# Optimization experiments

Hardware: AMD Instinct MI355X
Metric: run time of the kernel (lower is better)

Reference implementation:

```python
import jax, jax.numpy as jnp
import numpy as np

EPS = 1e-12  # torch F.normalize eps
NUM_HEADS = 4
DT = 0.25
NUM_STEPS = 4


def _l2norm(x, axis=-1):
    n = jnp.sqrt(jnp.sum(x * x, axis=axis, keepdims=True))
    return x / jnp.maximum(n, EPS)


def setup_inputs() -> dict:
    key = jax.random.key(0)
    k0, k1, k2, k3, k4 = jax.random.split(key, 5)
    B, T, D = 4, 2048, 256
    z = jax.random.normal(k0, (B, T, D), dtype=jnp.float32)
    omega = jax.random.normal(k1, (1, 1, D), dtype=jnp.float32) * 0.1
    Wqk = jax.random.normal(k2, (2 * D, D), dtype=jnp.float32) * (1.0 / np.sqrt(D))
    Wout = jax.random.normal(k3, (D, D), dtype=jnp.float32) * (1.0 / np.sqrt(D))
    bout = jax.random.normal(k4, (D,), dtype=jnp.float32) * 0.01
    return {"z": z, "omega": omega, "Wqk": Wqk, "Wout": Wout, "bout": bout}


def _kuramoto(x, omega, Wqk, Wout, bout):
    # x: [B, T, D]
    B, T, D = x.shape
    hd = D // NUM_HEADS
    qk = x @ Wqk.T  # [B, T, 2D]
    q, k = jnp.split(qk, 2, axis=-1)
    q = _l2norm(q.reshape(B, T, NUM_HEADS, hd))  # cosine-normalized per head
    k = _l2norm(k.reshape(B, T, NUM_HEADS, hd))
    # coupling: [B, H, T, T] cosine similarity
    coupling = jnp.einsum("bqhd,bkhd->bhqk", q, k)
    # sin nonlinearity replaces softmax
    force = jnp.einsum("bhqk,bkhd->bqhd", jnp.sin(coupling), k).reshape(B, T, D)
    return omega + force @ Wout.T + bout


def reference(z, omega, Wqk, Wout, bout):
    def f(x):
        return _kuramoto(x, omega, Wqk, Wout, bout)

    x = z
    for _ in range(NUM_STEPS):
        x = _l2norm(x)
        k1 = f(x)
        k2 = f(x + DT / 2 * k1)
        k3 = f(x + DT / 2 * k2)
        k4 = f(x + DT * k3)
        x = x + DT / 6 * (k1 + 2 * k2 + 2 * k3 + k4)
    return _l2norm(x)
```

## Files before the change

kernel.cpp:

```cpp
#include <hip/hip_runtime.h>
#include <cmath>

#define NB 4
#define TT 2048
#define DD 256
#define NH 4
#define BT (NB*TT)

static constexpr float DT_ = 0.25f;

typedef _Float16 f16x8 __attribute__((ext_vector_type(8)));
typedef _Float16 f16x4 __attribute__((ext_vector_type(4)));
typedef float    f32x4 __attribute__((ext_vector_type(4)));

static constexpr size_t HSZ = (size_t)NB * NH * TT * 64;
static constexpr size_t FSZ = (size_t)BT * 256;

__global__ __launch_bounds__(256)
void split_weights(const float* __restrict__ Wqk, const float* __restrict__ Wout,
                   _Float16* __restrict__ WqkH, _Float16* __restrict__ WqkL,
                   _Float16* __restrict__ WoutH, _Float16* __restrict__ WoutL)
{
    const int idx = blockIdx.x * 256 + threadIdx.x;
    const float4 v = (idx < 32768) ? ((const float4*)Wqk)[idx]
                                   : ((const float4*)Wout)[idx - 32768];
    f16x4 h, l;
    h[0]=(_Float16)v.x; l[0]=(_Float16)(v.x-(float)h[0]);
    h[1]=(_Float16)v.y; l[1]=(_Float16)(v.y-(float)h[1]);
    h[2]=(_Float16)v.z; l[2]=(_Float16)(v.z-(float)h[2]);
    h[3]=(_Float16)v.w; l[3]=(_Float16)(v.w-(float)h[3]);
    if (idx < 32768) { ((f16x4*)WqkH)[idx] = h; ((f16x4*)WqkL)[idx] = l; }
    else { ((f16x4*)WoutH)[idx-32768] = h; ((f16x4*)WoutL)[idx-32768] = l; }
}

__global__ __launch_bounds__(256)
void comb_weights(const float* __restrict__ Wqk, const float* __restrict__ Wout,
                  const float* __restrict__ omega, const float* __restrict__ bout,
                  _Float16* __restrict__ WcombH, _Float16* __restrict__ WcombL,
                  float* __restrict__ qkob)
{
    __shared__ float qrow[256];
    __shared__ float pr[256];
    const int n = blockIdx.x;
    const int k = threadIdx.x;
    qrow[k] = Wqk[n * 256 + k];
    __syncthreads();
    float s = 0.f;
    for (int m = 0; m < 256; ++m) s = fmaf(qrow[m], Wout[m * 256 + k], s);
    const _Float16 h = (_Float16)s;
    WcombH[n * 256 + k] = h;
    WcombL[n * 256 + k] = (_Float16)(s - (float)h);
    pr[k] = (omega[k] + bout[k]) * qrow[k];
    __syncthreads();
    if (k == 0) {
        float t = 0.f;
        for (int i = 0; i < 256; ++i) t += pr[i];
        qkob[n] = t;
    }
}

__global__ __launch_bounds__(256)
void l2norm_rows(const float* __restrict__ src, float* __restrict__ dst,
                 _Float16* __restrict__ dstH, _Float16* __restrict__ dstL) {
    const int wave = threadIdx.x >> 6;
    const int lane = threadIdx.x & 63;
    const size_t row = (size_t)blockIdx.x * 4 + wave;
    float4 v = ((const float4*)(src + row * DD))[lane];
    float ss = v.x*v.x + v.y*v.y + v.z*v.z + v.w*v.w;
    #pragma unroll
    for (int off = 32; off; off >>= 1) ss += __shfl_xor(ss, off, 64);
    const float inv = 1.0f / fmaxf(sqrtf(ss), 1e-12f);
    v.x *= inv; v.y *= inv; v.z *= inv; v.w *= inv;
    ((float4*)(dst + row * DD))[lane] = v;
    if (dstH != nullptr) {
        f16x4 h, l;
        h[0]=(_Float16)v.x; l[0]=(_Float16)(v.x-(float)h[0]);
        h[1]=(_Float16)v.y; l[1]=(_Float16)(v.y-(float)h[1]);
        h[2]=(_Float16)v.z; l[2]=(_Float16)(v.z-(float)h[2]);
        h[3]=(_Float16)v.w; l[3]=(_Float16)(v.w-(float)h[3]);
        ((f16x4*)(dstH + row * DD))[lane] = h;
        ((f16x4*)(dstL + row * DD))[lane] = l;
    }
}

__global__ __launch_bounds__(256)
void gemm_mfma(const _Float16* __restrict__ AH, const _Float16* __restrict__ AL,
               const float* __restrict__ Fp, float* __restrict__ Facc,
               const _Float16* __restrict__ BH, const _Float16* __restrict__ BL,
               float* __restrict__ qkx, const float* __restrict__ qkob,
               const float* __restrict__ omega, const float* __restrict__ bout,
               const float* __restrict__ xin, float* __restrict__ xout,
               _Float16* __restrict__ Qhi, _Float16* __restrict__ Qlo,
               _Float16* __restrict__ Khi, _Float16* __restrict__ Klo,
               _Float16* __restrict__ KtrH,
               int mode, float cc, int faccm)
{
    __shared__ _Float16 Ah[128 * 72];
    __shared__ _Float16 Al[128 * 72];
    __shared__ _Float16 Bh[64 * 72];
    __shared__ _Float16 Bl[64 * 72];
    const int m0 = blockIdx.x * 128, n0 = blockIdx.y * 64;
    const int t  = threadIdx.x;
    const int w  = t >> 6;
    const int l  = t & 63;
    const int lr = l & 15;
    const int lq = l >> 4;

    f32x4 acc[2][4];
    #pragma unroll
    for (int s = 0; s < 2; ++s)
        #pragma unroll
        for (int nt = 0; nt < 4; ++nt) acc[s][nt] = (f32x4){0.f,0.f,0.f,0.f};

    for (int kc = 0; kc < 4; ++kc) {
        const int k0 = kc * 64;
        __syncthreads();
        if (mode == 0) {
            #pragma unroll
            for (int s2 = 0; s2 < 4; ++s2) {
                const int idx = t + 256 * s2;
                const int r = idx >> 3, c8 = (idx & 7) * 8;
                *(uint4*)&Ah[r * 72 + c8] = *(const uint4*)(AH + (size_t)(m0 + r) * 256 + k0 + c8);
                *(uint4*)&Al[r * 72 + c8] = *(const uint4*)(AL + (size_t)(m0 + r) * 256 + k0 + c8);
            }
        } else {
            #pragma unroll
            for (int s2 = 0; s2 < 4; ++s2) {
                const int idx = t + 256 * s2;
                const int r = idx >> 3, c8 = (idx & 7) * 8;
                const size_t go = (size_t)(m0 + r) * 256 + k0 + c8;
                float sv[8] = {0,0,0,0,0,0,0,0};
                if (mode == 2) {
                    const float4 a0 = *(const float4*)(Facc + go);
                    const float4 a1 = *(const float4*)(Facc + go + 4);
                    sv[0]=a0.x; sv[1]=a0.y; sv[2]=a0.z; sv[3]=a0.w;
                    sv[4]=a1.x; sv[5]=a1.y; sv[6]=a1.z; sv[7]=a1.w;
                }
                #pragma unroll
                for (int p = 0; p < 3; ++p) {
                    const float4 a0 = *(const float4*)(Fp + p*FSZ + go);
                    const float4 a1 = *(const float4*)(Fp + p*FSZ + go + 4);
                    sv[0]+=a0.x; sv[1]+=a0.y; sv[2]+=a0.z; sv[3]+=a0.w;
                    sv[4]+=a1.x; sv[5]+=a1.y; sv[6]+=a1.z; sv[7]+=a1.w;
                }
                if (mode == 1 && blockIdx.y == 0) {
                    if (faccm == 1) {
                        *(float4*)(Facc + go)     = make_float4(sv[0], sv[1], sv[2], sv[3]);
                        *(float4*)(Facc + go + 4) = make_float4(sv[4], sv[5], sv[6], sv[7]);
                    } else {
                        float4 f0 = *(const float4*)(Facc + go);
                        float4 f1 = *(const float4*)(Facc + go + 4);
                        f0.x += 2.f*sv[0]; f0.y += 2.f*sv[1]; f0.z += 2.f*sv[2]; f0.w += 2.f*sv[3];
                        f1.x += 2.f*sv[4]; f1.y += 2.f*sv[5]; f1.z += 2.f*sv[6]; f1.w += 2.f*sv[7];
                        *(float4*)(Facc + go)     = f0;
                        *(float4*)(Facc + go + 4) = f1;
                    }
                }
                f16x8 hv, lv;
                #pragma unroll
                for (int e = 0; e < 8; ++e) {
                    hv[e] = (_Float16)sv[e];
                    lv[e] = (_Float16)(sv[e] - (float)hv[e]);
                }
                *(f16x8*)&Ah[r * 72 + c8] = hv;
                *(f16x8*)&Al[r * 72 + c8] = lv;
            }
        }
        #pragma unroll
        for (int s2 = 0; s2 < 2; ++s2) {
            const int idx = t + 256 * s2;
            const int r = idx >> 3, c8 = (idx & 7) * 8;
            *(uint4*)&Bh[r * 72 + c8] = *(const uint4*)(BH + (size_t)(n0 + r) * 256 + k0 + c8);
            *(uint4*)&Bl[r * 72 + c8] = *(const uint4*)(BL + (size_t)(n0 + r) * 256 + k0 + c8);
        }
        __syncthreads();
        #pragma unroll
        for (int c = 0; c < 2; ++c) {
            f16x8 ah[2], al[2], bh[4], bl[4];
            #pragma unroll
            for (int s = 0; s < 2; ++s) {
                ah[s] = *(const f16x8*)&Ah[(32*w + 16*s + lr) * 72 + 32*c + 8*lq];
                al[s] = *(const f16x8*)&Al[(32*w + 16*s + lr) * 72 + 32*c + 8*lq];
            }
            #pragma unroll
            for (int nt = 0; nt < 4; ++nt) {
                bh[nt] = *(const f16x8*)&Bh[(16*nt + lr) * 72 + 32*c + 8*lq];
                bl[nt] = *(const f16x8*)&Bl[(16*nt + lr) * 72 + 32*c + 8*lq];
            }
            #pragma unroll
            for (int s = 0; s < 2; ++s)
                #pragma unroll
                for (int nt = 0; nt < 4; ++nt) {
                    acc[s][nt] = __builtin_amdgcn_mfma_f32_16x16x32_f16(ah[s], bh[nt], acc[s][nt], 0, 0, 0);
                    acc[s][nt] = __builtin_amdgcn_mfma_f32_16x16x32_f16(ah[s], bl[nt], acc[s][nt], 0, 0, 0);
                    acc[s][nt] = __builtin_amdgcn_mfma_f32_16x16x32_f16(al[s], bh[nt], acc[s][nt], 0, 0, 0);
                }
        }
    }

    if (mode == 2) {
        #pragma unroll
        for (int s = 0; s < 2; ++s) {
            const int row0 = m0 + 32*w + 16*s + 4*lq;
            #pragma unroll
            for (int nt = 0; nt < 4; ++nt) {
                const int col = n0 + 16*nt + lr;
                const float ob = omega[col] + bout[col];
                #pragma unroll
                for (int r = 0; r < 4; ++r) {
                    const size_t off = (size_t)(row0 + r) * 256 + col;
                    xout[off] = xin[off] + (DT_ / 6.0f) * acc[s][nt][r] + DT_ * ob;
                }
            }
        }
    } else {
        float val[2][4][4];
        #pragma unroll
        for (int s = 0; s < 2; ++s) {
            const int row0 = m0 + 32*w + 16*s + 4*lq;
            #pragma unroll
            for (int nt = 0; nt < 4; ++nt) {
                const int col = n0 + 16*nt + lr;
                #pragma unroll
                for (int r = 0; r < 4; ++r) {
                    const size_t qo = (size_t)(row0 + r) * 512 + col;
                    if (mode == 0) {
                        val[s][nt][r] = acc[s][nt][r];
                        qkx[qo] = acc[s][nt][r];
                    } else {
                        val[s][nt][r] = qkx[qo] + cc * (acc[s][nt][r] + qkob[col]);
                    }
                }
            }
        }
        float ss[2][4];
        #pragma unroll
        for (int s = 0; s < 2; ++s)
            #pragma unroll
            for (int r = 0; r < 4; ++r) {
                float v = 0.f;
                #pragma unroll
                for (int nt = 0; nt < 4; ++nt) v += val[s][nt][r] * val[s][nt][r];
                ss[s][r] = v;
            }
        #pragma unroll
        for (int off = 1; off < 16; off <<= 1)
            #pragma unroll
            for (int s = 0; s < 2; ++s)
                #pragma unroll
                for (int r = 0; r < 4; ++r)
                    ss[s][r] += __shfl_xor(ss[s][r], off, 64);
        const int  b    = m0 >> 11;
        const int  h    = (n0 >> 6) & 3;
        const bool is_k = (n0 >= 256);
        const size_t bhi = (size_t)b * NH + h;
        _Float16* dhi = (is_k ? Khi : Qhi) + bhi * (size_t)TT * 64;
        _Float16* dlo = (is_k ? Klo : Qlo) + bhi * (size_t)TT * 64;
        const int mloc = m0 & (TT - 1);
        #pragma unroll
        for (int s = 0; s < 2; ++s) {
            const int r0 = 32*w + 16*s + 4*lq;
            float inv[4];
            #pragma unroll
            for (int r = 0; r < 4; ++r) inv[r] = 1.0f / fmaxf(sqrtf(ss[s][r]), 1e-12f);
            #pragma unroll
            for (int nt = 0; nt < 4; ++nt) {
                const int d = 16*nt + lr;
                f16x4 hv, lv;
                #pragma unroll
                for (int r = 0; r < 4; ++r) {
                    const float v2 = val[s][nt][r] * inv[r];
                    hv[r] = (_Float16)v2;
                    lv[r] = (_Float16)(v2 - (float)hv[r]);
                    dhi[(size_t)(mloc + r0 + r) * 64 + d] = hv[r];
                    dlo[(size_t)(mloc + r0 + r) * 64 + d] = lv[r];
                }
                if (is_k) {
                    const size_t tb = bhi * (size_t)64 * TT + (size_t)d * TT + mloc + r0;
                    *(f16x4*)(KtrH + tb) = hv;
                }
            }
        }
    }
}

__global__ __launch_bounds__(256, 3)
void kuramoto_attn(const _Float16* __restrict__ Qhi, const _Float16* __restrict__ Qlo,
                   const _Float16* __restrict__ Khi, const _Float16* __restrict__ Klo,
                   const _Float16* __restrict__ KtrH,
                   float* __restrict__ Fp)
{
    __shared__ _Float16 KjH[64 * 72];
    __shared__ _Float16 KjL[64 * 72];
    __shared__ _Float16 KdH[64 * 72];
    __shared__ _Float16 Pw[4][2][16 * 68];
    const int bh = blockIdx.z;
    const int b  = bh >> 2, h = bh & 3;
    const size_t base  = (size_t)bh * TT * 64;
    const size_t tbase = (size_t)bh * 64 * TT;
    const int t0 = blockIdx.y * 11;
    const int tn = (blockIdx.y == 2) ? 10 : 11;
    float* Fout = Fp + (size_t)blockIdx.y * FSZ;
    const int t = threadIdx.x;
    const int w = t >> 6;
    const int l = t & 63;
    const int lr = l & 15;
    const int lq = l >> 4;
    const int i0 = blockIdx.x * 128 + w * 32;

    f16x8 qh[2][2], ql[2][2];
    #pragma unroll
    for (int s = 0; s < 2; ++s) {
        const size_t qoff = base + (size_t)(i0 + 16*s + lr) * 64 + lq * 8;
        qh[s][0] = *(const f16x8*)(Qhi + qoff);
        qh[s][1] = *(const f16x8*)(Qhi + qoff + 32);
        ql[s][0] = *(const f16x8*)(Qlo + qoff);
        ql[s][1] = *(const f16x8*)(Qlo + qoff + 32);
    }

    f32x4 Facc[2][4];
    #pragma unroll
    for (int s = 0; s < 2; ++s)
        #pragma unroll
        for (int nt = 0; nt < 4; ++nt) Facc[s][nt] = (f32x4){0.f, 0.f, 0.f, 0.f};

    const int sr = t >> 3;
    const int so = (t & 7) * 8;

    for (int tt = 0; tt < tn; ++tt) {
        const int j0 = (t0 + tt) * 64;
        __syncthreads();
        {
            *(uint4*)&KjH[sr * 72 + so]        = *(const uint4*)(Khi + base + (size_t)(j0 + sr) * 64 + so);
            *(uint4*)&KjH[(sr + 32) * 72 + so] = *(const uint4*)(Khi + base + (size_t)(j0 + sr + 32) * 64 + so);
            *(uint4*)&KjL[sr * 72 + so]        = *(const uint4*)(Klo + base + (size_t)(j0 + sr) * 64 + so);
            *(uint4*)&KjL[(sr + 32) * 72 + so] = *(const uint4*)(Klo + base + (size_t)(j0 + sr + 32) * 64 + so);
            *(uint4*)&KdH[sr * 72 + so]        = *(const uint4*)(KtrH + tbase + (size_t)sr * TT + j0 + so);
            *(uint4*)&KdH[(sr + 32) * 72 + so] = *(const uint4*)(KtrH + tbase + (size_t)(sr + 32) * TT + j0 + so);
        }
        __syncthreads();
        #pragma unroll
        for (int nt = 0; nt < 4; ++nt) {
            f16x8 kh0 = *(const f16x8*)&KjH[(16*nt + lr) * 72 + lq * 8];
            f16x8 kh1 = *(const f16x8*)&KjH[(16*nt + lr) * 72 + 32 + lq * 8];
            f16x8 kl0 = *(const f16x8*)&KjL[(16*nt + lr) * 72 + lq * 8];
            f16x8 kl1 = *(const f16x8*)&KjL[(16*nt + lr) * 72 + 32 + lq * 8];
            #pragma unroll
            for (int s = 0; s < 2; ++s) {
                f32x4 a = (f32x4){0.f, 0.f, 0.f, 0.f};
                a = __builtin_amdgcn_mfma_f32_16x16x32_f16(kh0, qh[s][0], a, 0, 0, 0);
                a = __builtin_amdgcn_mfma_f32_16x16x32_f16(kh1, qh[s][1], a, 0, 0, 0);
                a = __builtin_amdgcn_mfma_f32_16x16x32_f16(kl0, qh[s][0], a, 0, 0, 0);
                a = __builtin_amdgcn_mfma_f32_16x16x32_f16(kl1, qh[s][1], a, 0, 0, 0);
                a = __builtin_amdgcn_mfma_f32_16x16x32_f16(kh0, ql[s][0], a, 0, 0, 0);
                a = __builtin_amdgcn_mfma_f32_16x16x32_f16(kh1, ql[s][1], a, 0, 0, 0);
                f16x4 pv;
                #pragma unroll
                for (int r = 0; r < 4; ++r) pv[r] = (_Float16)__sinf(a[r]);
                *(f16x4*)&Pw[w][s][lr * 68 + 16*nt + 4*lq] = pv;
            }
        }
        f16x8 ph[2][2];
        #pragma unroll
        for (int s = 0; s < 2; ++s) {
            ph[s][0] = *(const f16x8*)&Pw[w][s][lr * 68 + lq * 8];
            ph[s][1] = *(const f16x8*)&Pw[w][s][lr * 68 + 32 + lq * 8];
        }
        #pragma unroll
        for (int nt = 0; nt < 4; ++nt) {
            f16x8 kh0 = *(const f16x8*)&KdH[(16*nt + lr) * 72 + lq * 8];
            f16x8 kh1 = *(const f16x8*)&KdH[(16*nt + lr) * 72 + 32 + lq * 8];
            #pragma unroll
            for (int s = 0; s < 2; ++s) {
                Facc[s][nt] = __builtin_amdgcn_mfma_f32_16x16x32_f16(ph[s][0], kh0, Facc[s][nt], 0, 0, 0);
                Facc[s][nt] = __builtin_amdgcn_mfma_f32_16x16x32_f16(ph[s][1], kh1, Facc[s][nt], 0, 0, 0);
            }
        }
    }
    #pragma unroll
    for (int s = 0; s < 2; ++s) {
        float* fo = Fout + ((size_t)b * TT + i0 + 16*s + 4*lq) * 256 + h * 64 + lr;
        #pragma unroll
        for (int nt = 0; nt < 4; ++nt)
            #pragma unroll
            for (int r = 0; r < 4; ++r)
                fo[(size_t)r * 256 + nt * 16] = Facc[s][nt][r];
    }
}

extern "C" void kernel_launch(void* const* d_in, const int* in_sizes, int n_in,
                              void* d_out, int out_size, void* d_ws, size_t ws_size,
                              hipStream_t stream) {
    const float* z     = (const float*)d_in[0];
    const float* omega = (const float*)d_in[1];
    const float* Wqk   = (const float*)d_in[2];
    const float* Wout  = (const float*)d_in[3];
    const float* bout  = (const float*)d_in[4];

    float* x    = (float*)d_ws;
    float* Facc = x + FSZ;
    float* Fp   = Facc + FSZ;
    float* qkx  = Fp + 3 * FSZ;
    float* qkob = qkx + (size_t)BT * 512;
    _Float16* xsH  = (_Float16*)(qkob + 512);
    _Float16* xsL  = xsH  + FSZ;
    _Float16* Qhi  = xsL  + FSZ;
    _Float16* Qlo  = Qhi  + HSZ;
    _Float16* Khi  = Qlo  + HSZ;
    _Float16* Klo  = Khi  + HSZ;
    _Float16* KtrH = Klo  + HSZ;
    _Float16* WqkH = KtrH + HSZ;
    _Float16* WqkL = WqkH + (size_t)512 * 256;
    _Float16* WoutH= WqkL + (size_t)512 * 256;
    _Float16* WoutL= WoutH + (size_t)256 * 256;
    _Float16* WcombH = WoutL + (size_t)256 * 256;
    _Float16* WcombL = WcombH + (size_t)512 * 256;

    split_weights<<<192, 256, 0, stream>>>(Wqk, Wout, WqkH, WqkL, WoutH, WoutL);
    comb_weights<<<512, 256, 0, stream>>>(Wqk, Wout, omega, bout, WcombH, WcombL, qkob);

    for (int step = 0; step < 4; ++step) {
        l2norm_rows<<<BT / 4, 256, 0, stream>>>(step == 0 ? z : x, x, xsH, xsL);
        gemm_mfma<<<dim3(BT / 128, 8), 256, 0, stream>>>(
            xsH, xsL, nullptr, nullptr, WqkH, WqkL, qkx, nullptr,
            nullptr, nullptr, nullptr, nullptr,
            Qhi, Qlo, Khi, Klo, KtrH, 0, 0.f, 0);
        kuramoto_attn<<<dim3(TT / 128, 3, NB * NH), 256, 0, stream>>>(
            Qhi, Qlo, Khi, Klo, KtrH, Fp);
        for (int s = 1; s <= 3; ++s) {
            const float cs = (s == 3) ? 0.25f : 0.125f;
            gemm_mfma<<<dim3(BT / 128, 8), 256, 0, stream>>>(
                nullptr, nullptr, Fp, Facc, WcombH, WcombL, qkx, qkob,
                nullptr, nullptr, nullptr, nullptr,
                Qhi, Qlo, Khi, Klo, KtrH, 1, cs, (s == 1) ? 1 : 2);
            kuramoto_attn<<<dim3(TT / 128, 3, NB * NH), 256, 0, stream>>>(
                Qhi, Qlo, Khi, Klo, KtrH, Fp);
        }
        gemm_mfma<<<dim3(BT / 128, 4), 256, 0, stream>>>(
            nullptr, nullptr, Fp, Facc, WoutH, WoutL, nullptr, nullptr,
            omega, bout, x, x,
            nullptr, nullptr, nullptr, nullptr, nullptr, 2, 0.f, 0);
    }
    l2norm_rows<<<BT / 4, 256, 0, stream>>>(x, (float*)d_out, nullptr, nullptr);
}
```

Before: 1.196 ms.

## Enlarge attention query tile to 64 rows per wave with four key splits

Each wave in the attention kernel now handles 64 query rows instead of 32, so every K tile staged in shared memory is reused across twice as many queries. The key range is split four ways instead of three, with a matching fourth partial buffer in the workspace and in the downstream reduction. The sin-probability staging buffer is shrunk and reused per query subtile, and the KdH fragments are hoisted into registers. Register use rises, so the occupancy hint drops from 3 to 2 blocks, and the grid shrinks to 8x4x16 blocks, which may underfill the GPU.

```diff
diff --git a/kernel.cpp b/kernel.cpp
--- a/kernel.cpp
+++ b/kernel.cpp
@@ -137,7 +137,7 @@
                     sv[4]=a1.x; sv[5]=a1.y; sv[6]=a1.z; sv[7]=a1.w;
                 }
                 #pragma unroll
-                for (int p = 0; p < 3; ++p) {
+                for (int p = 0; p < 4; ++p) {
                     const float4 a0 = *(const float4*)(Fp + p*FSZ + go);
                     const float4 a1 = *(const float4*)(Fp + p*FSZ + go + 4);
                     sv[0]+=a0.x; sv[1]+=a0.y; sv[2]+=a0.z; sv[3]+=a0.w;
@@ -284,7 +284,7 @@
     }
 }
 
-__global__ __launch_bounds__(256, 3)
+__global__ __launch_bounds__(256, 2)
 void kuramoto_attn(const _Float16* __restrict__ Qhi, const _Float16* __restrict__ Qlo,
                    const _Float16* __restrict__ Khi, const _Float16* __restrict__ Klo,
                    const _Float16* __restrict__ KtrH,
@@ -293,24 +293,23 @@
     __shared__ _Float16 KjH[64 * 72];
     __shared__ _Float16 KjL[64 * 72];
     __shared__ _Float16 KdH[64 * 72];
-    __shared__ _Float16 Pw[4][2][16 * 68];
+    __shared__ _Float16 Pw[4][16 * 68];
     const int bh = blockIdx.z;
     const int b  = bh >> 2, h = bh & 3;
     const size_t base  = (size_t)bh * TT * 64;
     const size_t tbase = (size_t)bh * 64 * TT;
-    const int t0 = blockIdx.y * 11;
-    const int tn = (blockIdx.y == 2) ? 10 : 11;
+    const int j00 = blockIdx.y * 512;
     float* Fout = Fp + (size_t)blockIdx.y * FSZ;
     const int t = threadIdx.x;
     const int w = t >> 6;
     const int l = t & 63;
     const int lr = l & 15;
     const int lq = l >> 4;
-    const int i0 = blockIdx.x * 128 + w * 32;
-
-    f16x8 qh[2][2], ql[2][2];
+    const int i0 = blockIdx.x * 256 + w * 64;
+
+    f16x8 qh[4][2], ql[4][2];
     #pragma unroll
-    for (int s = 0; s < 2; ++s) {
+    for (int s = 0; s < 4; ++s) {
         const size_t qoff = base + (size_t)(i0 + 16*s + lr) * 64 + lq * 8;
         qh[s][0] = *(const f16x8*)(Qhi + qoff);
         qh[s][1] = *(const f16x8*)(Qhi + qoff + 32);
@@ -318,17 +317,17 @@
         ql[s][1] = *(const f16x8*)(Qlo + qoff + 32);
     }
 
-    f32x4 Facc[2][4];
+    f32x4 Facc[4][4];
     #pragma unroll
-    for (int s = 0; s < 2; ++s)
+    for (int s = 0; s < 4; ++s)
         #pragma unroll
         for (int nt = 0; nt < 4; ++nt) Facc[s][nt] = (f32x4){0.f, 0.f, 0.f, 0.f};
 
     const int sr = t >> 3;
     const int so = (t & 7) * 8;
 
-    for (int tt = 0; tt < tn; ++tt) {
-        const int j0 = (t0 + tt) * 64;
+    for (int tt = 0; tt < 8; ++tt) {
+        const int j0 = j00 + tt * 64;
         __syncthreads();
         {
             *(uint4*)&KjH[sr * 72 + so]        = *(const uint4*)(Khi + base + (size_t)(j0 + sr) * 64 + so);
@@ -339,6 +338,7 @@
             *(uint4*)&KdH[(sr + 32) * 72 + so] = *(const uint4*)(KtrH + tbase + (size_t)(sr + 32) * TT + j0 + so);
         }
         __syncthreads();
+        f16x4 pv[4][4];
         #pragma unroll
         for (int nt = 0; nt < 4; ++nt) {
             f16x8 kh0 = *(const f16x8*)&KjH[(16*nt + lr) * 72 + lq * 8];
@@ -346,7 +346,7 @@
             f16x8 kl0 = *(const f16x8*)&KjL[(16*nt + lr) * 72 + lq * 8];
             f16x8 kl1 = *(const f16x8*)&KjL[(16*nt + lr) * 72 + 32 + lq * 8];
             #pragma unroll
-            for (int s = 0; s < 2; ++s) {
+            for (int s = 0; s < 4; ++s) {
                 f32x4 a = (f32x4){0.f, 0.f, 0.f, 0.f};
                 a = __builtin_amdgcn_mfma_f32_16x16x32_f16(kh0, qh[s][0], a, 0, 0, 0);
                 a = __builtin_amdgcn_mfma_f32_16x16x32_f16(kh1, qh[s][1], a, 0, 0, 0);
@@ -354,31 +354,32 @@
                 a = __builtin_amdgcn_mfma_f32_16x16x32_f16(kl1, qh[s][1], a, 0, 0, 0);
                 a = __builtin_amdgcn_mfma_f32_16x16x32_f16(kh0, ql[s][0], a, 0, 0, 0);
                 a = __builtin_amdgcn_mfma_f32_16x16x32_f16(kh1, ql[s][1], a, 0, 0, 0);
-                f16x4 pv;
-                #pragma unroll
-                for (int r = 0; r < 4; ++r) pv[r] = (_Float16)__sinf(a[r]);
-                *(f16x4*)&Pw[w][s][lr * 68 + 16*nt + 4*lq] = pv;
-            }
-        }
-        f16x8 ph[2][2];
-        #pragma unroll
-        for (int s = 0; s < 2; ++s) {
-            ph[s][0] = *(const f16x8*)&Pw[w][s][lr * 68 + lq * 8];
-            ph[s][1] = *(const f16x8*)&Pw[w][s][lr * 68 + 32 + lq * 8];
-        }
+                #pragma unroll
+                for (int r = 0; r < 4; ++r) pv[s][nt][r] = (_Float16)__sinf(a[r]);
+            }
+        }
+        f16x8 kd0[4], kd1[4];
         #pragma unroll
         for (int nt = 0; nt < 4; ++nt) {
-            f16x8 kh0 = *(const f16x8*)&KdH[(16*nt + lr) * 72 + lq * 8];
-            f16x8 kh1 = *(const f16x8*)&KdH[(16*nt + lr) * 72 + 32 + lq * 8];
-            #pragma unroll
-            for (int s = 0; s < 2; ++s) {
-                Facc[s][nt] = __builtin_amdgcn_mfma_f32_16x16x32_f16(ph[s][0], kh0, Facc[s][nt], 0, 0, 0);
-                Facc[s][nt] = __builtin_amdgcn_mfma_f32_16x16x32_f16(ph[s][1], kh1, Facc[s][nt], 0, 0, 0);
+            kd0[nt] = *(const f16x8*)&KdH[(16*nt + lr) * 72 + lq * 8];
+            kd1[nt] = *(const f16x8*)&KdH[(16*nt + lr) * 72 + 32 + lq * 8];
+        }
+        #pragma unroll
+        for (int s = 0; s < 4; ++s) {
+            #pragma unroll
+            for (int nt = 0; nt < 4; ++nt)
+                *(f16x4*)&Pw[w][lr * 68 + 16*nt + 4*lq] = pv[s][nt];
+            f16x8 ph0 = *(const f16x8*)&Pw[w][lr * 68 + lq * 8];
+            f16x8 ph1 = *(const f16x8*)&Pw[w][lr * 68 + 32 + lq * 8];
+            #pragma unroll
+            for (int nt = 0; nt < 4; ++nt) {
+                Facc[s][nt] = __builtin_amdgcn_mfma_f32_16x16x32_f16(ph0, kd0[nt], Facc[s][nt], 0, 0, 0);
+                Facc[s][nt] = __builtin_amdgcn_mfma_f32_16x16x32_f16(ph1, kd1[nt], Facc[s][nt], 0, 0, 0);
             }
         }
     }
     #pragma unroll
-    for (int s = 0; s < 2; ++s) {
+    for (int s = 0; s < 4; ++s) {
         float* fo = Fout + ((size_t)b * TT + i0 + 16*s + 4*lq) * 256 + h * 64 + lr;
         #pragma unroll
         for (int nt = 0; nt < 4; ++nt)
@@ -400,7 +401,7 @@
     float* x    = (float*)d_ws;
     float* Facc = x + FSZ;
     float* Fp   = Facc + FSZ;
-    float* qkx  = Fp + 3 * FSZ;
+    float* qkx  = Fp + 4 * FSZ;
     float* qkob = qkx + (size_t)BT * 512;
     _Float16* xsH  = (_Float16*)(qkob + 512);
     _Float16* xsL  = xsH  + FSZ;
@@ -425,7 +426,7 @@
             xsH, xsL, nullptr, nullptr, WqkH, WqkL, qkx, nullptr,
             nullptr, nullptr, nullptr, nullptr,
             Qhi, Qlo, Khi, Klo, KtrH, 0, 0.f, 0);
-        kuramoto_attn<<<dim3(TT / 128, 3, NB * NH), 256, 0, stream>>>(
+        kuramoto_attn<<<dim3(TT / 256, 4, NB * NH), 256, 0, stream>>>(
             Qhi, Qlo, Khi, Klo, KtrH, Fp);
         for (int s = 1; s <= 3; ++s) {
             const float cs = (s == 3) ? 0.25f : 0.125f;
@@ -433,7 +434,7 @@
                 nullptr, nullptr, Fp, Facc, WcombH, WcombL, qkx, qkob,
                 nullptr, nullptr, nullptr, nullptr,
                 Qhi, Qlo, Khi, Klo, KtrH, 1, cs, (s == 1) ? 1 : 2);
-            kuramoto_attn<<<dim3(TT / 128, 3, NB * NH), 256, 0, stream>>>(
+            kuramoto_attn<<<dim3(TT / 256, 4, NB * NH), 256, 0, stream>>>(
                 Qhi, Qlo, Khi, Klo, KtrH, Fp);
         }
         gemm_mfma<<<dim3(BT / 128, 4), 256, 0, stream>>>(
```

After: 1.264 ms. 1.06x slower.
